# Kernel optimization log

Measured on AMD Instinct MI355X. Metric: run time of the kernel, lower is better.

The kernel has to match this reference:

```python
import jax, jax.numpy as jnp
import numpy as np

NH = 12
LEVEL = 4  # Lmin = 2**LEVEL = 16


def _build_sets(T, Lmin):
    l_list, r_list = [], []
    L = Lmin
    while L <= T:
        for i in range(T // L):
            l_list.append(i * L)
            r_list.append((i + 1) * L - 1)
        L *= 2
    return np.asarray(l_list, np.int32), np.asarray(r_list, np.int32)


def _get_slice(x_cum, l_idx, r_idx):
    # x_cum: [B,nh,T,hs]; returns inclusive range-sums x[l..r] via cumsum diffs
    r = x_cum[:, :, r_idx, :]
    l = x_cum[:, :, np.maximum(np.asarray(l_idx) - 1, 0), :]
    mask = (np.asarray(l_idx) >= 1).astype(x_cum.dtype)[None, None, :, None]
    return r - l * mask


def _get_slice_dyn(x_cum, l_idx, r_idx):
    # same but with traced/jnp indices (tail term)
    r = x_cum[:, :, r_idx, :]
    l = x_cum[:, :, jnp.maximum(l_idx - 1, 0), :]
    mask = (l_idx >= 1).astype(x_cum.dtype)[None, None, :, None]
    return r - l * mask


def setup_inputs() -> dict:
    key = jax.random.key(0)
    k0, k1, k2, k3 = jax.random.split(key, 4)
    B, T, C = 8, 2048, 768
    hs = C // NH
    s = 0.02
    return {
        "x": jax.random.normal(k0, (B, T, C), jnp.float32),
        "Wqkv": jax.random.normal(k1, (3 * C, C), jnp.float32) * s,
        "Wproj": jax.random.normal(k2, (C, C), jnp.float32) * s,
        "Wv": jax.random.normal(k3, (hs, hs * hs), jnp.float32) * s,
        "bv": jnp.zeros((hs,), jnp.float32),
    }


def reference(x, Wqkv, Wproj, Wv, bv):
    B, T, C = x.shape
    nh = NH
    hs = C // nh
    Lmin = 2 ** LEVEL
    scale = 1.0 / jnp.sqrt(jnp.asarray(hs, x.dtype))

    qkv = x @ Wqkv.T  # [B,T,3C]
    q, k, v0 = jnp.split(qkv, 3, axis=-1)
    q = q.reshape(B, T, nh, hs).transpose(0, 2, 1, 3)   # [B,nh,T,hs]
    k = k.reshape(B, T, nh, hs).transpose(0, 2, 1, 3)
    v0 = v0.reshape(B, T, nh, hs).transpose(0, 2, 1, 3)

    # v = v_proj(outer(k, v0).flatten)  == einsum with Wv reshaped [hs,hs,hs]
    Wv3 = Wv.reshape(hs, hs, hs)
    v = jnp.einsum('bhti,bhtj,eij->bhte', k, v0, Wv3) + bv

    k_cum = jnp.cumsum(k, axis=2)
    v_cum = jnp.cumsum(v, axis=2)

    l_idx, r_idx = _build_sets(T, Lmin)  # static dyadic sets
    K = _get_slice(k_cum, l_idx, r_idx)  # [B,nh,S,hs]
    V = _get_slice(v_cum, l_idx, r_idx)

    t_idx = jnp.arange(T)
    mask = t_idx[:, None] >= jnp.asarray(r_idx)[None, :]  # [T,S]
    logits = jnp.einsum('bhtd,bhsd->bhts', q, K) * scale
    logits = jnp.where(mask[None, None], logits, -jnp.inf)

    # tail: remainder within the current Lmin block
    l_tail = (t_idx // Lmin) * Lmin
    K_tail = _get_slice_dyn(k_cum, l_tail, t_idx)  # [B,nh,T,hs]
    V_tail = _get_slice_dyn(v_cum, l_tail, t_idx)
    tail_logits = jnp.sum(q * K_tail, axis=-1) * scale  # [B,nh,T]

    att = jax.nn.softmax(jnp.concatenate([logits, tail_logits[..., None]], axis=-1), axis=-1)
    out = jnp.einsum('bhts,bhsd->bhtd', att[..., :-1], V) + att[..., -1:] * V_tail
    out = out.transpose(0, 2, 1, 3).reshape(B, T, C)
    return out @ Wproj.T
```

## Files before the change

### kernel.cpp

```cpp
#include <hip/hip_runtime.h>


typedef float  f32x4  __attribute__((ext_vector_type(4)));
typedef _Float16 half8 __attribute__((ext_vector_type(8)));
typedef _Float16 half4 __attribute__((ext_vector_type(4)));

#define DEV __device__ __forceinline__
#define MFMA16(a, b, c) __builtin_amdgcn_mfma_f32_16x16x32_f16((a), (b), (c), 0, 0, 0)
#define GLOAD16(gp, lp)                                                  \
  __builtin_amdgcn_global_load_lds(                                      \
      (const __attribute__((address_space(1))) unsigned int*)(gp),       \
      (__attribute__((address_space(3))) unsigned int*)(lp), 16, 0, 0)

__global__ __launch_bounds__(256) void k_cast16(const float* __restrict__ in,
                                                _Float16* __restrict__ outh, int n4) {
  int i = blockIdx.x * 256 + threadIdx.x;
  if (i >= n4) return;
  f32x4 v = ((const f32x4*)in)[i];
  half4 o;
#pragma unroll
  for (int c = 0; c < 4; ++c) o[c] = (_Float16)v[c];
  ((half4*)outh)[i] = o;
}

__global__ __launch_bounds__(256, 3) void k_gemm_qkv(
    const _Float16* __restrict__ A16, const _Float16* __restrict__ B16,
    _Float16* __restrict__ qo, _Float16* __restrict__ ko, _Float16* __restrict__ v0o) {
  __shared__ _Float16 sA[128][64], sB[128][64];
  const int K = 768;
  int tid = threadIdx.x, lane = tid & 63, wave = tid >> 6;
  int l15 = lane & 15, g = lane >> 4;
  int wr = wave >> 1, wc = wave & 1;
  int wg = (blockIdx.x & 7) * 288 + (blockIdx.x >> 3);
  int n0 = (wg % 18) * 128, m0 = (wg / 18) * 128;
  f32x4 acc[4][4];
#pragma unroll
  for (int a = 0; a < 4; ++a)
#pragma unroll
    for (int b = 0; b < 4; ++b) acc[a][b] = f32x4{0.f, 0.f, 0.f, 0.f};
  int rsel = lane >> 3;
  int csel = (lane & 7) ^ rsel;
  for (int k0 = 0; k0 < K; k0 += 64) {
#pragma unroll
    for (int r = 0; r < 4; ++r) {
      int row = wave * 32 + r * 8 + rsel;
      GLOAD16(&A16[(size_t)(m0 + row) * K + k0 + csel * 8], &sA[wave * 32 + r * 8][0]);
      GLOAD16(&B16[(size_t)(n0 + row) * K + k0 + csel * 8], &sB[wave * 32 + r * 8][0]);
    }
    __syncthreads();
#pragma unroll
    for (int kk = 0; kk < 2; ++kk) {
      int kc = kk * 4 + g;
      int cc = ((kc ^ (l15 & 7)) << 3);
      half8 af[4], bf[4];
#pragma unroll
      for (int mf = 0; mf < 4; ++mf) af[mf] = *(const half8*)&sA[wr * 64 + mf * 16 + l15][cc];
#pragma unroll
      for (int nf = 0; nf < 4; ++nf) bf[nf] = *(const half8*)&sB[wc * 64 + nf * 16 + l15][cc];
#pragma unroll
      for (int mf = 0; mf < 4; ++mf)
#pragma unroll
        for (int nf = 0; nf < 4; ++nf)
          acc[mf][nf] = MFMA16(af[mf], bf[nf], acc[mf][nf]);
    }
    __syncthreads();
  }
  int sec = n0 / 768;
  int nb = n0 - sec * 768;
#pragma unroll
  for (int mf = 0; mf < 4; ++mf)
#pragma unroll
    for (int nf = 0; nf < 4; ++nf)
#pragma unroll
      for (int r = 0; r < 4; ++r) {
        int m = m0 + wr * 64 + mf * 16 + (g << 2) + r;
        int n = nb + wc * 64 + nf * 16 + l15;
        int b = m >> 11, t = m & 2047;
        int h = n >> 6, d = n & 63;
        size_t idx = (((size_t)b * 12 + h) * 2048 + t) * 64 + d;
        _Float16 val = (_Float16)acc[mf][nf][r];
        if (sec == 0) qo[idx] = val;
        else if (sec == 1) ko[idx] = val;
        else v0o[idx] = val;
      }
}

__global__ __launch_bounds__(256, 3) void k_veins(
    const _Float16* __restrict__ kh, const _Float16* __restrict__ v0g,
    const _Float16* __restrict__ Wvh, const float* __restrict__ bv,
    _Float16* __restrict__ vout) {
  __shared__ _Float16 ks[256][72];
  __shared__ _Float16 sB[2][64][64];
  int tid = threadIdx.x, lane = tid & 63, wave = tid >> 6;
  int l15 = lane & 15, g = lane >> 4, g8 = g << 3;
  size_t row0 = (size_t)blockIdx.x * 256;

  int srow_lo = wave * 8 + (lane >> 3);
  int scsrc = (lane & 7) ^ (lane >> 3);
  auto STAGE = [&](int b, int i) {
#pragma unroll
    for (int h = 0; h < 2; ++h) {
      GLOAD16(&Wvh[(size_t)(h * 32 + srow_lo) * 4096 + i * 64 + (scsrc << 3)],
              ((_Float16*)sB) + (size_t)b * 4096 + (h * 256 + wave * 64) * 8);
    }
  };

#pragma unroll
  for (int r = 0; r < 8; ++r) {
    int row = (tid >> 3) + r * 32;
    int c8 = (tid & 7) << 3;
    *(half8*)&ks[row][c8] = *(const half8*)&kh[(row0 + row) * 64 + c8];
  }
  half8 v0r[4][2];
#pragma unroll
  for (int mf = 0; mf < 4; ++mf) {
    size_t rb = (row0 + wave * 64 + mf * 16 + l15) * 64;
#pragma unroll
    for (int kk = 0; kk < 2; ++kk)
      v0r[mf][kk] = *(const half8*)&v0g[rb + kk * 32 + g8];
  }
  f32x4 acc[4][4];
#pragma unroll
  for (int a = 0; a < 4; ++a)
#pragma unroll
    for (int b = 0; b < 4; ++b) acc[a][b] = f32x4{0.f, 0.f, 0.f, 0.f};

  STAGE(0, 0);
  __syncthreads();
  int r0 = wave * 64 + l15;
  for (int i8 = 0; i8 < 8; ++i8) {
    half8 kr0 = *(const half8*)&ks[r0][i8 * 8];
    half8 kr1 = *(const half8*)&ks[r0 + 16][i8 * 8];
    half8 kr2 = *(const half8*)&ks[r0 + 32][i8 * 8];
    half8 kr3 = *(const half8*)&ks[r0 + 48][i8 * 8];
#pragma unroll
    for (int ii = 0; ii < 8; ++ii) {
      int i = i8 * 8 + ii;
      int cur = i & 1;
      if (i < 63) STAGE(cur ^ 1, i + 1);
      half8 b0[4], b1[4];
#pragma unroll
      for (int nf = 0; nf < 4; ++nf) {
        b0[nf] = *(const half8*)&sB[cur][nf * 16 + l15][((g ^ (l15 & 7)) << 3)];
        b1[nf] = *(const half8*)&sB[cur][nf * 16 + l15][(((4 + g) ^ (l15 & 7)) << 3)];
      }
      _Float16 kv0 = kr0[ii], kv1 = kr1[ii], kv2 = kr2[ii], kv3 = kr3[ii];
      {
        half8 a0 = v0r[0][0] * kv0, a1 = v0r[1][0] * kv1;
        half8 a2 = v0r[2][0] * kv2, a3 = v0r[3][0] * kv3;
#pragma unroll
        for (int nf = 0; nf < 4; ++nf) {
          acc[0][nf] = MFMA16(a0, b0[nf], acc[0][nf]);
          acc[1][nf] = MFMA16(a1, b0[nf], acc[1][nf]);
          acc[2][nf] = MFMA16(a2, b0[nf], acc[2][nf]);
          acc[3][nf] = MFMA16(a3, b0[nf], acc[3][nf]);
        }
      }
      {
        half8 a0 = v0r[0][1] * kv0, a1 = v0r[1][1] * kv1;
        half8 a2 = v0r[2][1] * kv2, a3 = v0r[3][1] * kv3;
#pragma unroll
        for (int nf = 0; nf < 4; ++nf) {
          acc[0][nf] = MFMA16(a0, b1[nf], acc[0][nf]);
          acc[1][nf] = MFMA16(a1, b1[nf], acc[1][nf]);
          acc[2][nf] = MFMA16(a2, b1[nf], acc[2][nf]);
          acc[3][nf] = MFMA16(a3, b1[nf], acc[3][nf]);
        }
      }
      __syncthreads();
    }
  }
#pragma unroll
  for (int mf = 0; mf < 4; ++mf)
#pragma unroll
    for (int nf = 0; nf < 4; ++nf) {
      int e = (nf << 4) + l15;
      float bve = bv[e];
#pragma unroll
      for (int r = 0; r < 4; ++r) {
        int row = wave * 64 + mf * 16 + (g << 2) + r;
        vout[(row0 + row) * 64 + e] = (_Float16)(acc[mf][nf][r] + bve);
      }
    }
}

__global__ __launch_bounds__(256) void k_segments(
    const _Float16* __restrict__ kmat, const _Float16* __restrict__ vmat,
    _Float16* __restrict__ Ks, _Float16* __restrict__ Vt) {
  __shared__ float Ls[255][64];
  int bh = blockIdx.x, tid = threadIdx.x;
  size_t bh2048 = (size_t)bh * 2048;
  for (int task = tid; task < 8192; task += 256) {
    int seg = task >> 6, d = task & 63;
    const _Float16* p = kmat + (bh2048 + seg * 16) * 64 + d;
    float s = 0.f;
#pragma unroll
    for (int u = 0; u < 16; ++u) s += (float)p[u * 64];
    Ls[seg][d] = s;
  }
  __syncthreads();
  {
    int bprev = 0, bcur = 128, cnt = 64;
    for (int lev = 1; lev < 8; ++lev) {
      for (int task = tid; task < cnt * 64; task += 256) {
        int i = task >> 6, d = task & 63;
        Ls[bcur + i][d] = Ls[bprev + 2 * i][d] + Ls[bprev + 2 * i + 1][d];
      }
      __syncthreads();
      bprev = bcur; bcur += cnt; cnt >>= 1;
    }
  }
  for (int task = tid; task < 16384; task += 256) {
    int seg = task >> 6;
    float v = (seg < 255) ? Ls[seg][task & 63] : 0.f;
    Ks[(size_t)bh * 16384 + task] = (_Float16)v;
  }
  __syncthreads();
  for (int task = tid; task < 8192; task += 256) {
    int seg = task >> 6, d = task & 63;
    const _Float16* p = vmat + (bh2048 + seg * 16) * 64 + d;
    float s = 0.f;
#pragma unroll
    for (int u = 0; u < 16; ++u) s += (float)p[u * 64];
    Ls[seg][d] = s;
  }
  __syncthreads();
  {
    int bprev = 0, bcur = 128, cnt = 64;
    for (int lev = 1; lev < 8; ++lev) {
      for (int task = tid; task < cnt * 64; task += 256) {
        int i = task >> 6, d = task & 63;
        Ls[bcur + i][d] = Ls[bprev + 2 * i][d] + Ls[bprev + 2 * i + 1][d];
      }
      __syncthreads();
      bprev = bcur; bcur += cnt; cnt >>= 1;
    }
  }
  for (int task = tid; task < 16384; task += 256) {
    int d = task >> 8, seg = task & 255;
    float v = (seg < 255) ? Ls[seg][d] : 0.f;
    Vt[(size_t)bh * 16384 + task] = (_Float16)v;
  }
}

__global__ __launch_bounds__(256) void k_attn2(
    const _Float16* __restrict__ qm, const _Float16* __restrict__ km,
    const _Float16* __restrict__ vm,
    const _Float16* __restrict__ Ks, const _Float16* __restrict__ Vt,
    _Float16* __restrict__ outp) {
  __shared__ __align__(16) _Float16 P[4][16][280];
  __shared__ __align__(16) _Float16 tK[4][16][72];
  __shared__ __align__(16) _Float16 tV[4][16][72];
  int tid = threadIdx.x, lane = tid & 63, wave = tid >> 6;
  int orig = blockIdx.y * 32 + blockIdx.x;
  int wg = (orig & 7) * 384 + (orig >> 3);
  int tile = wg & 31, bh = wg >> 5;
  int t0 = tile * 64, tw0 = t0 + wave * 16;
  size_t bh2048 = (size_t)bh * 2048;
  int l15 = lane & 15, g = lane >> 4, g8 = g << 3;

  {
    const _Float16* kp = km + (bh2048 + tw0) * 64 + lane;
    const _Float16* vp = vm + (bh2048 + tw0) * 64 + lane;
    float ka = 0.f, va = 0.f;
#pragma unroll
    for (int t = 0; t < 16; ++t) {
      ka += (float)kp[t * 64];
      va += (float)vp[t * 64];
      tK[wave][t][lane] = (_Float16)ka;
      tV[wave][t][lane] = (_Float16)va;
    }
  }
  half8 qf[2];
  {
    const _Float16* qp = qm + (bh2048 + tw0 + l15) * 64 + g8;
    qf[0] = *(const half8*)qp;
    qf[1] = *(const half8*)(qp + 32);
  }
  unsigned mA = 0, mE = 0;
#pragma unroll
  for (int nf = 0; nf < 16; ++nf) {
    int seg = nf * 16 + l15;
    if (seg < 255) {
      int m = 256 - seg;
      int cl = 32 - __clz(m - 1);
      int lev = 8 - cl;
      int rdx = (seg - (256 - (256 >> lev)) + 1) * (16 << lev) - 1;
      if (rdx < tw0) mA |= 1u << nf;
      else if (rdx == tw0 + 15) mE |= 1u << nf;
    }
  }
  unsigned mAny = mA | mE;
  unsigned pmask = 0;
#pragma unroll
  for (int ks = 0; ks < 8; ++ks)
    if (__any((int)((mAny >> (2 * ks)) & 3u))) pmask |= 1u << ks;

  f32x4 acc[17];
#pragma unroll
  for (int i = 0; i < 17; ++i) acc[i] = f32x4{0.f, 0.f, 0.f, 0.f};
  const _Float16* KsB = Ks + (size_t)bh * 16384;
  __builtin_amdgcn_s_setprio(1);
#pragma unroll
  for (int ks = 0; ks < 8; ++ks) {
    if ((pmask >> ks) & 1) {
      const _Float16* ph = KsB + (size_t)(ks * 32 + l15) * 64 + g8;
      half8 h00 = *(const half8*)ph;
      half8 h01 = *(const half8*)(ph + 32);
      half8 h10 = *(const half8*)(ph + 1024);
      half8 h11 = *(const half8*)(ph + 1056);
      acc[2 * ks] = MFMA16(qf[0], h00, acc[2 * ks]);
      acc[2 * ks] = MFMA16(qf[1], h01, acc[2 * ks]);
      acc[2 * ks + 1] = MFMA16(qf[0], h10, acc[2 * ks + 1]);
      acc[2 * ks + 1] = MFMA16(qf[1], h11, acc[2 * ks + 1]);
    }
  }
  {
    const _Float16* tp = &tK[wave][l15][g8];
    half8 t0f = *(const half8*)tp;
    half8 t1f = *(const half8*)(tp + 32);
    acc[16] = MFMA16(qf[0], t0f, acc[16]);
    acc[16] = MFMA16(qf[1], t1f, acc[16]);
  }
  __builtin_amdgcn_s_setprio(0);

  const float c = 0.125f * 1.44269504f;
  float mx[4], sm[4], et[4];
#pragma unroll
  for (int r = 0; r < 4; ++r) {
    int tr = g * 4 + r;
    mx[r] = (l15 == tr) ? acc[16][r] * c : -3.0e38f;
  }
#pragma unroll
  for (int nf = 0; nf < 16; ++nf) {
    bool bA = (mA >> nf) & 1, bE = (mE >> nf) & 1;
#pragma unroll
    for (int r = 0; r < 4; ++r) {
      bool u = bA || (bE && g == 3 && r == 3);
      if (u) mx[r] = fmaxf(mx[r], acc[nf][r] * c);
    }
  }
#pragma unroll
  for (int off = 1; off < 16; off <<= 1)
#pragma unroll
    for (int r = 0; r < 4; ++r) mx[r] = fmaxf(mx[r], __shfl_xor(mx[r], off));
#pragma unroll
  for (int r = 0; r < 4; ++r) {
    int tr = g * 4 + r;
    et[r] = (l15 == tr) ? exp2f(acc[16][r] * c - mx[r]) : 0.f;
    sm[r] = et[r];
  }
#pragma unroll
  for (int ks = 0; ks < 8; ++ks) {
    if ((pmask >> ks) & 1) {
#pragma unroll
      for (int f = 0; f < 2; ++f) {
        int nf = 2 * ks + f;
        bool bA = (mA >> nf) & 1, bE = (mE >> nf) & 1;
#pragma unroll
        for (int r = 0; r < 4; ++r) {
          bool u = bA || (bE && g == 3 && r == 3);
          float e = u ? exp2f(acc[nf][r] * c - mx[r]) : 0.f;
          acc[nf][r] = e;
          sm[r] += e;
        }
      }
    }
  }
#pragma unroll
  for (int off = 1; off < 16; off <<= 1)
#pragma unroll
    for (int r = 0; r < 4; ++r) sm[r] += __shfl_xor(sm[r], off);
  float inv[4];
#pragma unroll
  for (int r = 0; r < 4; ++r) inv[r] = 1.f / sm[r];

  {
    half4 z4 = {};
    *(half4*)&P[wave][lane >> 2][256 + (lane & 3) * 4] = z4;
  }
#pragma unroll
  for (int nf = 0; nf < 16; ++nf)
#pragma unroll
    for (int r = 0; r < 4; ++r)
      P[wave][g * 4 + r][nf * 16 + l15] = (_Float16)(acc[nf][r] * inv[r]);
#pragma unroll
  for (int r = 0; r < 4; ++r)
    if (l15 == g * 4 + r) P[wave][l15][256 + l15] = (_Float16)(et[r] * inv[r]);

  f32x4 oa[4];
#pragma unroll
  for (int i = 0; i < 4; ++i) oa[i] = f32x4{0.f, 0.f, 0.f, 0.f};
  const _Float16* VB = Vt + (size_t)bh * 16384;
  __builtin_amdgcn_s_setprio(1);
#pragma unroll
  for (int ks = 0; ks < 8; ++ks) {
    if ((pmask >> ks) & 1) {
      half8 pa = *(const half8*)&P[wave][l15][ks * 32 + g8];
#pragma unroll
      for (int n2 = 0; n2 < 4; ++n2) {
        half8 vb = *(const half8*)(VB + (size_t)(n2 * 16 + l15) * 256 + ks * 32 + g8);
        oa[n2] = MFMA16(pa, vb, oa[n2]);
      }
    }
  }
  {
    half8 pa = *(const half8*)&P[wave][l15][256 + (g & 1) * 8];
#pragma unroll
    for (int n2 = 0; n2 < 4; ++n2) {
      half8 vt = {};
      if (g < 2) {
#pragma unroll
        for (int jj = 0; jj < 8; ++jj) vt[jj] = tV[wave][g8 + jj][n2 * 16 + l15];
      }
      oa[n2] = MFMA16(pa, vt, oa[n2]);
    }
  }
  __builtin_amdgcn_s_setprio(0);
  int b = bh / 12, h = bh - b * 12;
  size_t obase = ((size_t)b * 2048 + tw0) * 768 + h * 64;
#pragma unroll
  for (int n2 = 0; n2 < 4; ++n2)
#pragma unroll
    for (int r = 0; r < 4; ++r)
      outp[obase + (size_t)(g * 4 + r) * 768 + n2 * 16 + l15] = (_Float16)oa[n2][r];
}

__global__ __launch_bounds__(256, 3) void k_gemm_proj(
    const _Float16* __restrict__ A16, const _Float16* __restrict__ B16,
    float* __restrict__ C) {
  __shared__ _Float16 sA[128][64], sB[128][64];
  const int K = 768;
  int tid = threadIdx.x, lane = tid & 63, wave = tid >> 6;
  int l15 = lane & 15, g = lane >> 4;
  int wr = wave >> 1, wc = wave & 1;
  int wg = (blockIdx.x & 7) * 96 + (blockIdx.x >> 3);
  int n0 = (wg % 6) * 128, m0 = (wg / 6) * 128;
  f32x4 acc[4][4];
#pragma unroll
  for (int a = 0; a < 4; ++a)
#pragma unroll
    for (int b = 0; b < 4; ++b) acc[a][b] = f32x4{0.f, 0.f, 0.f, 0.f};
  int rsel = lane >> 3;
  int csel = (lane & 7) ^ rsel;
  for (int k0 = 0; k0 < K; k0 += 64) {
#pragma unroll
    for (int r = 0; r < 4; ++r) {
      int row = wave * 32 + r * 8 + rsel;
      GLOAD16(&A16[(size_t)(m0 + row) * K + k0 + csel * 8], &sA[wave * 32 + r * 8][0]);
      GLOAD16(&B16[(size_t)(n0 + row) * K + k0 + csel * 8], &sB[wave * 32 + r * 8][0]);
    }
    __syncthreads();
#pragma unroll
    for (int kk = 0; kk < 2; ++kk) {
      int kc = kk * 4 + g;
      int cc = ((kc ^ (l15 & 7)) << 3);
      half8 af[4], bf[4];
#pragma unroll
      for (int mf = 0; mf < 4; ++mf) af[mf] = *(const half8*)&sA[wr * 64 + mf * 16 + l15][cc];
#pragma unroll
      for (int nf = 0; nf < 4; ++nf) bf[nf] = *(const half8*)&sB[wc * 64 + nf * 16 + l15][cc];
#pragma unroll
      for (int mf = 0; mf < 4; ++mf)
#pragma unroll
        for (int nf = 0; nf < 4; ++nf)
          acc[mf][nf] = MFMA16(af[mf], bf[nf], acc[mf][nf]);
    }
    __syncthreads();
  }
#pragma unroll
  for (int mf = 0; mf < 4; ++mf)
#pragma unroll
    for (int nf = 0; nf < 4; ++nf)
#pragma unroll
      for (int r = 0; r < 4; ++r) {
        int m = m0 + wr * 64 + mf * 16 + (g << 2) + r;
        int n = n0 + wc * 64 + nf * 16 + l15;
        C[(size_t)m * 768 + n] = acc[mf][nf][r];
      }
}

extern "C" void kernel_launch(void* const* d_in, const int* in_sizes, int n_in,
                              void* d_out, int out_size, void* d_ws, size_t ws_size,
                              hipStream_t stream) {
  const float* x = (const float*)d_in[0];
  const float* Wqkv = (const float*)d_in[1];
  const float* Wproj = (const float*)d_in[2];
  const float* Wv = (const float*)d_in[3];
  const float* bv = (const float*)d_in[4];
  float* out = (float*)d_out;
  char* ws = (char*)d_ws;
  size_t off = 0;
  auto alloc = [&](size_t bytes) -> void* {
    void* p = (void*)(ws + off);
    off += (bytes + 255) & ~(size_t)255;
    return p;
  };
  _Float16* x16  = (_Float16*)alloc(12582912ull * 2);
  _Float16* wq16 = (_Float16*)alloc(1769472ull * 2);
  _Float16* wv16 = (_Float16*)alloc(262144ull * 2 + 8192);
  _Float16* wp16 = (_Float16*)alloc(589824ull * 2);
  _Float16* q16  = (_Float16*)alloc(12582912ull * 2);
  _Float16* k16  = (_Float16*)alloc(12582912ull * 2);
  _Float16* v016 = (_Float16*)alloc(12582912ull * 2);
  _Float16* vm16 = (_Float16*)alloc(12582912ull * 2);
  _Float16* Ks   = (_Float16*)alloc(1572864ull * 2);
  _Float16* Vt   = (_Float16*)alloc(1572864ull * 2);
  _Float16* outp = (_Float16*)alloc(12582912ull * 2);

  k_cast16<<<dim3(12288), dim3(256), 0, stream>>>(x, x16, 3145728);
  k_cast16<<<dim3(1728), dim3(256), 0, stream>>>(Wqkv, wq16, 442368);
  k_cast16<<<dim3(256), dim3(256), 0, stream>>>(Wv, wv16, 65536);
  k_cast16<<<dim3(576), dim3(256), 0, stream>>>(Wproj, wp16, 147456);
  k_gemm_qkv<<<dim3(2304), dim3(256), 0, stream>>>(x16, wq16, q16, k16, v016);
  k_veins<<<dim3(768), dim3(256), 0, stream>>>(k16, v016, wv16, bv, vm16);
  k_segments<<<dim3(96), dim3(256), 0, stream>>>(k16, vm16, Ks, Vt);
  k_attn2<<<dim3(32, 96), dim3(256), 0, stream>>>(q16, k16, vm16, Ks, Vt, outp);
  k_gemm_proj<<<dim3(768), dim3(256), 0, stream>>>(outp, wp16, out);
}
```

Baseline: 340.4 us.

## Prefetch all K and V segment fragments into registers, drop per-tile skip mask

Removes the wave-level pmask that skipped segment tiles with no causal contribution, so every wave now always loads and multiplies all eight key/value segment chunks. All K fragments are issued up front before the QK MFMAs, and the V fragments are loaded early, half before the softmax and half after writing P, so the global-load latency overlaps with compute. Launch bounds now request two blocks per SM. The cost is extra loads and MFMAs for early query tiles that previously skipped work, plus heavy register use (about 64 half8 prefetch registers) that the occupancy hint may turn into spills.

```diff
diff --git a/kernel.cpp b/kernel.cpp
--- a/kernel.cpp
+++ b/kernel.cpp
@@ -243,7 +243,7 @@
   }
 }
 
-__global__ __launch_bounds__(256) void k_attn2(
+__global__ __launch_bounds__(256, 2) void k_attn2(
     const _Float16* __restrict__ qm, const _Float16* __restrict__ km,
     const _Float16* __restrict__ vm,
     const _Float16* __restrict__ Ks, const _Float16* __restrict__ Vt,
@@ -290,30 +290,43 @@
       else if (rdx == tw0 + 15) mE |= 1u << nf;
     }
   }
-  unsigned mAny = mA | mE;
-  unsigned pmask = 0;
-#pragma unroll
-  for (int ks = 0; ks < 8; ++ks)
-    if (__any((int)((mAny >> (2 * ks)) & 3u))) pmask |= 1u << ks;
 
   f32x4 acc[17];
 #pragma unroll
   for (int i = 0; i < 17; ++i) acc[i] = f32x4{0.f, 0.f, 0.f, 0.f};
   const _Float16* KsB = Ks + (size_t)bh * 16384;
+  half8 hf[4][4], hg[4][4];
+#pragma unroll
+  for (int ksl = 0; ksl < 4; ++ksl) {
+    const _Float16* ph = KsB + (size_t)(ksl * 32 + l15) * 64 + g8;
+    hf[ksl][0] = *(const half8*)ph;
+    hf[ksl][1] = *(const half8*)(ph + 32);
+    hf[ksl][2] = *(const half8*)(ph + 1024);
+    hf[ksl][3] = *(const half8*)(ph + 1056);
+  }
+#pragma unroll
+  for (int ksl = 0; ksl < 4; ++ksl) {
+    const _Float16* ph = KsB + (size_t)((ksl + 4) * 32 + l15) * 64 + g8;
+    hg[ksl][0] = *(const half8*)ph;
+    hg[ksl][1] = *(const half8*)(ph + 32);
+    hg[ksl][2] = *(const half8*)(ph + 1024);
+    hg[ksl][3] = *(const half8*)(ph + 1056);
+  }
   __builtin_amdgcn_s_setprio(1);
 #pragma unroll
-  for (int ks = 0; ks < 8; ++ks) {
-    if ((pmask >> ks) & 1) {
-      const _Float16* ph = KsB + (size_t)(ks * 32 + l15) * 64 + g8;
-      half8 h00 = *(const half8*)ph;
-      half8 h01 = *(const half8*)(ph + 32);
-      half8 h10 = *(const half8*)(ph + 1024);
-      half8 h11 = *(const half8*)(ph + 1056);
-      acc[2 * ks] = MFMA16(qf[0], h00, acc[2 * ks]);
-      acc[2 * ks] = MFMA16(qf[1], h01, acc[2 * ks]);
-      acc[2 * ks + 1] = MFMA16(qf[0], h10, acc[2 * ks + 1]);
-      acc[2 * ks + 1] = MFMA16(qf[1], h11, acc[2 * ks + 1]);
-    }
+  for (int ksl = 0; ksl < 4; ++ksl) {
+    acc[2 * ksl]     = MFMA16(qf[0], hf[ksl][0], acc[2 * ksl]);
+    acc[2 * ksl]     = MFMA16(qf[1], hf[ksl][1], acc[2 * ksl]);
+    acc[2 * ksl + 1] = MFMA16(qf[0], hf[ksl][2], acc[2 * ksl + 1]);
+    acc[2 * ksl + 1] = MFMA16(qf[1], hf[ksl][3], acc[2 * ksl + 1]);
+  }
+#pragma unroll
+  for (int ksl = 0; ksl < 4; ++ksl) {
+    int nf = 2 * (ksl + 4);
+    acc[nf]     = MFMA16(qf[0], hg[ksl][0], acc[nf]);
+    acc[nf]     = MFMA16(qf[1], hg[ksl][1], acc[nf]);
+    acc[nf + 1] = MFMA16(qf[0], hg[ksl][2], acc[nf + 1]);
+    acc[nf + 1] = MFMA16(qf[1], hg[ksl][3], acc[nf + 1]);
   }
   {
     const _Float16* tp = &tK[wave][l15][g8];
@@ -324,6 +337,14 @@
   }
   __builtin_amdgcn_s_setprio(0);
 
+  const _Float16* VB = Vt + (size_t)bh * 16384;
+  half8 vta[4][4];
+#pragma unroll
+  for (int ksl = 0; ksl < 4; ++ksl)
+#pragma unroll
+    for (int n2 = 0; n2 < 4; ++n2)
+      vta[ksl][n2] = *(const half8*)(VB + (size_t)(n2 * 16 + l15) * 256 + ksl * 32 + g8);
+
   const float c = 0.125f * 1.44269504f;
   float mx[4], sm[4], et[4];
 #pragma unroll
@@ -351,20 +372,14 @@
     sm[r] = et[r];
   }
 #pragma unroll
-  for (int ks = 0; ks < 8; ++ks) {
-    if ((pmask >> ks) & 1) {
-#pragma unroll
-      for (int f = 0; f < 2; ++f) {
-        int nf = 2 * ks + f;
-        bool bA = (mA >> nf) & 1, bE = (mE >> nf) & 1;
-#pragma unroll
-        for (int r = 0; r < 4; ++r) {
-          bool u = bA || (bE && g == 3 && r == 3);
-          float e = u ? exp2f(acc[nf][r] * c - mx[r]) : 0.f;
-          acc[nf][r] = e;
-          sm[r] += e;
-        }
-      }
+  for (int nf = 0; nf < 16; ++nf) {
+    bool bA = (mA >> nf) & 1, bE = (mE >> nf) & 1;
+#pragma unroll
+    for (int r = 0; r < 4; ++r) {
+      bool u = bA || (bE && g == 3 && r == 3);
+      float e = u ? exp2f(acc[nf][r] * c - mx[r]) : 0.f;
+      acc[nf][r] = e;
+      sm[r] += e;
     }
   }
 #pragma unroll
@@ -388,21 +403,29 @@
   for (int r = 0; r < 4; ++r)
     if (l15 == g * 4 + r) P[wave][l15][256 + l15] = (_Float16)(et[r] * inv[r]);
 
+  half8 vtb[4][4];
+#pragma unroll
+  for (int ksl = 0; ksl < 4; ++ksl)
+#pragma unroll
+    for (int n2 = 0; n2 < 4; ++n2)
+      vtb[ksl][n2] = *(const half8*)(VB + (size_t)(n2 * 16 + l15) * 256 + (ksl + 4) * 32 + g8);
   f32x4 oa[4];
 #pragma unroll
   for (int i = 0; i < 4; ++i) oa[i] = f32x4{0.f, 0.f, 0.f, 0.f};
-  const _Float16* VB = Vt + (size_t)bh * 16384;
   __builtin_amdgcn_s_setprio(1);
 #pragma unroll
-  for (int ks = 0; ks < 8; ++ks) {
-    if ((pmask >> ks) & 1) {
-      half8 pa = *(const half8*)&P[wave][l15][ks * 32 + g8];
-#pragma unroll
-      for (int n2 = 0; n2 < 4; ++n2) {
-        half8 vb = *(const half8*)(VB + (size_t)(n2 * 16 + l15) * 256 + ks * 32 + g8);
-        oa[n2] = MFMA16(pa, vb, oa[n2]);
-      }
-    }
+  for (int ksl = 0; ksl < 4; ++ksl) {
+    half8 pa = *(const half8*)&P[wave][l15][ksl * 32 + g8];
+#pragma unroll
+    for (int n2 = 0; n2 < 4; ++n2)
+      oa[n2] = MFMA16(pa, vta[ksl][n2], oa[n2]);
+  }
+#pragma unroll
+  for (int ksl = 0; ksl < 4; ++ksl) {
+    half8 pa = *(const half8*)&P[wave][l15][(ksl + 4) * 32 + g8];
+#pragma unroll
+    for (int n2 = 0; n2 < 4; ++n2)
+      oa[n2] = MFMA16(pa, vtb[ksl][n2], oa[n2]);
   }
   {
     half8 pa = *(const half8*)&P[wave][l15][256 + (g & 1) * 8];
```

After: 345.5 us. Within noise of the previous version (+1.5%).
